# Performance work log

Hardware: AMD Instinct MI355X
Metric: run time of the kernel (lower is better)

The kernel has to match this reference:

```python
import jax, jax.numpy as jnp
import numpy as np

B, S, HID = 4, 512, 768
NH, HD = 12, 64          # num_heads, head_size = HID // NH
REL = 64                 # rel_dim
NEG_INF = -1e9


def setup_inputs() -> dict:
    key = jax.random.key(0)
    ks = jax.random.split(key, 12)
    input_tensor = jax.random.normal(ks[0], (B, S, HID), jnp.float32)
    graph_matrix = (jax.random.uniform(ks[1], (B, S, S)) < 0.3).astype(jnp.float32)
    # end_mask: one-hot at the last position (null attention slot)
    end_mask = jnp.zeros((B, S), jnp.float32).at[:, S - 1].set(1.0)
    rel_embeddings = jax.random.normal(ks[2], (B, S, S, REL), jnp.float32)
    w = lambda k, shp: jax.random.normal(k, shp, jnp.float32) * 0.02
    return {
        "input_tensor": input_tensor,
        "graph_matrix": graph_matrix,
        "end_mask": end_mask,
        "rel_embeddings": rel_embeddings,
        "Wq": w(ks[3], (HID, HID)), "bq": jnp.zeros((HID,), jnp.float32),
        "Wk": w(ks[4], (HID, HID)), "bk": jnp.zeros((HID,), jnp.float32),
        "Wv": w(ks[5], (HID, HID)), "bv": jnp.zeros((HID,), jnp.float32),
        "Wr": w(ks[6], (REL, HD)), "br": jnp.zeros((HD,), jnp.float32),
    }


def reference(input_tensor, graph_matrix, end_mask, rel_embeddings,
              Wq, bq, Wk, bk, Wv, bv, Wr, br):
    # use_null_att_pos: allow attending to the end/null slot
    g = graph_matrix + end_mask[:, None, :]              # (B,S,S)
    neg_inf_mask = (1.0 - g) * NEG_INF                   # (B,S,S)

    def heads(x):  # (B,S,HID) -> (B,NH,S,HD)
        return x.reshape(B, S, NH, HD).transpose(0, 2, 1, 3)

    q = heads(input_tensor @ Wq + bq)
    k = heads(input_tensor @ Wk + bk)
    v = heads(input_tensor @ Wv + bv)

    rel = rel_embeddings @ Wr + br                       # (B,S,S,HD), shared over heads
    # matmul_rel: (x_i * (y_j + z_ij)).sum(-1) = q.k^T + q.rel, per head
    scores = (jnp.einsum('bhid,bhjd->bhij', q, k)
              + jnp.einsum('bhid,bijd->bhij', q, rel))   # (B,NH,S,S)
    scores = scores / jnp.sqrt(jnp.float32(HD)) + neg_inf_mask[:, None]
    probs = jax.nn.softmax(scores, axis=-1)              # dropout p=0 -> identity

    ctx = jnp.einsum('bhij,bhjd->bhid', probs, v)        # (B,NH,S,HD)
    return ctx.transpose(0, 2, 1, 3).reshape(B, S, NH * HD)
```

## Files before the change

### kernel.cpp

```cpp
#include <hip/hip_runtime.h>
#include <hip/hip_bf16.h>
#include <hip/hip_fp16.h>
#include <cstddef>
#include <cstdint>

typedef __attribute__((ext_vector_type(8))) short bf16x8;
typedef __attribute__((ext_vector_type(4))) float f32x4;

#define MFMA16(a, b, c) __builtin_amdgcn_mfma_f32_16x16x32_bf16((a), (b), (c), 0, 0, 0)

static constexpr int B = 4, S = 512, HID = 768, NH = 12, HD = 64;
static constexpr int QKV_N = B * NH * S * HD;
static constexpr size_t SCORES_N = (size_t)B * NH * S * S;

__device__ __forceinline__ short f2bf(float f) {
  unsigned u = __builtin_bit_cast(unsigned, f);
  u += 0x7FFFu + ((u >> 16) & 1u);
  return (short)(u >> 16);
}
__device__ __forceinline__ float h2f(short s) {
  __half h = __builtin_bit_cast(__half, (unsigned short)s);
  return __half2float(h);
}
__device__ __forceinline__ bf16x8 ld_cvt8(const float* __restrict__ p) {
  float4 a = *reinterpret_cast<const float4*>(p);
  float4 b = *reinterpret_cast<const float4*>(p + 4);
  bf16x8 r;
  r[0] = f2bf(a.x); r[1] = f2bf(a.y); r[2] = f2bf(a.z); r[3] = f2bf(a.w);
  r[4] = f2bf(b.x); r[5] = f2bf(b.y); r[6] = f2bf(b.z); r[7] = f2bf(b.w);
  return r;
}
__device__ __forceinline__ f32x4 ld4nt(const float* p) {
  return __builtin_nontemporal_load(reinterpret_cast<const f32x4*>(p));
}
__device__ __forceinline__ bf16x8 cvt8(f32x4 a, f32x4 b) {
  bf16x8 r;
  r[0] = f2bf(a[0]); r[1] = f2bf(a[1]); r[2] = f2bf(a[2]); r[3] = f2bf(a[3]);
  r[4] = f2bf(b[0]); r[5] = f2bf(b[1]); r[6] = f2bf(b[2]); r[7] = f2bf(b[3]);
  return r;
}

__global__ __launch_bounds__(256) void k_qkv(
    const float* __restrict__ x,
    const float* __restrict__ Wq, const float* __restrict__ bq,
    const float* __restrict__ Wk, const float* __restrict__ bk,
    const float* __restrict__ Wv, const float* __restrict__ bv,
    const float* __restrict__ Wr,
    short* __restrict__ qkv, short* __restrict__ qrb, short* __restrict__ vT) {
  __shared__ short As[64 * 40];
  __shared__ short Bs[64 * 40];
  __shared__ short qs[64 * 72];
  const int m0 = blockIdx.x * 64;
  const int nt = blockIdx.y;
  const int mat = nt / 12;
  const int nc0 = (nt % 12) * 64;
  const float* __restrict__ W    = (mat == 0) ? Wq : (mat == 1) ? Wk : Wv;
  const float* __restrict__ bias = (mat == 0) ? bq : (mat == 1) ? bk : bv;
  short* __restrict__ outp = qkv + (size_t)mat * QKV_N;
  const int t = threadIdx.x;
  const int w = t >> 6, lane = t & 63;
  const int wm = (w >> 1) * 32, wn = (w & 1) * 32;
  const int lr = lane & 15, lk = lane >> 4;
  f32x4 acc[2][2] = {};
  for (int kk = 0; kk < 768; kk += 32) {
#pragma unroll
    for (int it = 0; it < 2; ++it) {
      int f = it * 256 + t;
      {
        int r = f >> 3, c4 = f & 7;
        float4 v = *reinterpret_cast<const float4*>(x + (size_t)(m0 + r) * 768 + kk + c4 * 4);
        short* d = &As[r * 40 + c4 * 4];
        d[0] = f2bf(v.x); d[1] = f2bf(v.y); d[2] = f2bf(v.z); d[3] = f2bf(v.w);
      }
      {
        int kr = f >> 4, c4 = f & 15;
        float4 v = *reinterpret_cast<const float4*>(W + (size_t)(kk + kr) * 768 + nc0 + c4 * 4);
        int c = c4 * 4;
        Bs[(c + 0) * 40 + kr] = f2bf(v.x);
        Bs[(c + 1) * 40 + kr] = f2bf(v.y);
        Bs[(c + 2) * 40 + kr] = f2bf(v.z);
        Bs[(c + 3) * 40 + kr] = f2bf(v.w);
      }
    }
    __syncthreads();
    bf16x8 a0 = *reinterpret_cast<const bf16x8*>(&As[(wm + lr) * 40 + lk * 8]);
    bf16x8 a1 = *reinterpret_cast<const bf16x8*>(&As[(wm + 16 + lr) * 40 + lk * 8]);
    bf16x8 b0 = *reinterpret_cast<const bf16x8*>(&Bs[(wn + lr) * 40 + lk * 8]);
    bf16x8 b1 = *reinterpret_cast<const bf16x8*>(&Bs[(wn + 16 + lr) * 40 + lk * 8]);
    acc[0][0] = MFMA16(a0, b0, acc[0][0]);
    acc[0][1] = MFMA16(a0, b1, acc[0][1]);
    acc[1][0] = MFMA16(a1, b0, acc[1][0]);
    acc[1][1] = MFMA16(a1, b1, acc[1][1]);
    __syncthreads();
  }
  const int b_ = m0 >> 9;
  if (mat == 2) {
#pragma unroll
    for (int mf = 0; mf < 2; ++mf)
#pragma unroll
      for (int nf = 0; nf < 2; ++nf) {
        int col = nc0 + wn + nf * 16 + lr;
        float bv_ = bias[col];
        int h = col >> 6, d = col & 63;
#pragma unroll
        for (int reg = 0; reg < 4; ++reg) {
          int j = (m0 + wm + mf * 16 + lk * 4 + reg) & 511;
          vT[((size_t)(b_ * NH + h) * HD + d) * S + j] = f2bf(acc[mf][nf][reg] + bv_);
        }
      }
    return;
  }
#pragma unroll
  for (int mf = 0; mf < 2; ++mf)
#pragma unroll
    for (int nf = 0; nf < 2; ++nf) {
      int col = nc0 + wn + nf * 16 + lr;
      float bv_ = bias[col];
      int h = col >> 6, d = col & 63;
#pragma unroll
      for (int reg = 0; reg < 4; ++reg) {
        int mloc = wm + mf * 16 + lk * 4 + reg;
        int i = (m0 + mloc) & 511;
        short qv = f2bf(acc[mf][nf][reg] + bv_);
        outp[(size_t)((b_ * NH + h) * S + i) * HD + d] = qv;
        if (mat == 0) qs[mloc * 72 + d] = qv;
      }
    }
  if (mat == 0) {
    const int h0 = nc0 >> 6;
    __syncthreads();
    f32x4 qacc[2][2] = {};
#pragma unroll
    for (int ks = 0; ks < 2; ++ks) {
      int k0 = ks * 32 + lk * 8;
      bf16x8 a0 = *reinterpret_cast<const bf16x8*>(&qs[(wm + lr) * 72 + k0]);
      bf16x8 a1 = *reinterpret_cast<const bf16x8*>(&qs[(wm + 16 + lr) * 72 + k0]);
      bf16x8 b0 = ld_cvt8(Wr + (size_t)(wn + lr) * 64 + k0);
      bf16x8 b1 = ld_cvt8(Wr + (size_t)(wn + 16 + lr) * 64 + k0);
      qacc[0][0] = MFMA16(a0, b0, qacc[0][0]);
      qacc[0][1] = MFMA16(a0, b1, qacc[0][1]);
      qacc[1][0] = MFMA16(a1, b0, qacc[1][0]);
      qacc[1][1] = MFMA16(a1, b1, qacc[1][1]);
    }
#pragma unroll
    for (int mf = 0; mf < 2; ++mf)
#pragma unroll
      for (int nf = 0; nf < 2; ++nf) {
        int r = wn + nf * 16 + lr;
#pragma unroll
        for (int reg = 0; reg < 4; ++reg) {
          int i = (m0 + wm + mf * 16 + lk * 4 + reg) & 511;
          qrb[((size_t)(b_ * NH + h0) * S + i) * 64 + r] = f2bf(qacc[mf][nf][reg] * 0.125f);
        }
      }
  }
}

__global__ __launch_bounds__(256) void k_qk(const short* __restrict__ q,
                                            const short* __restrict__ kmat,
                                            const float* __restrict__ graph,
                                            const float* __restrict__ endm,
                                            __half* __restrict__ sc) {
  const int j0 = blockIdx.x * 64, i0 = blockIdx.y * 64;
  const int bh = blockIdx.z;
  const int b = bh / NH, hh = bh % NH;
  const short* __restrict__ qp = q + (size_t)(bh * S) * HD;
  const short* __restrict__ kp = kmat + (size_t)(bh * S) * HD;
  const int t = threadIdx.x;
  const int w = t >> 6, lane = t & 63;
  const int wm = (w >> 1) * 32, wn = (w & 1) * 32;
  const int lr = lane & 15, lk = lane >> 4;
  f32x4 acc[2][2] = {};
#pragma unroll
  for (int ks = 0; ks < 2; ++ks) {
    int k0 = ks * 32 + lk * 8;
    bf16x8 a0 = *reinterpret_cast<const bf16x8*>(qp + (size_t)(i0 + wm + lr) * 64 + k0);
    bf16x8 a1 = *reinterpret_cast<const bf16x8*>(qp + (size_t)(i0 + wm + 16 + lr) * 64 + k0);
    bf16x8 b0 = *reinterpret_cast<const bf16x8*>(kp + (size_t)(j0 + wn + lr) * 64 + k0);
    bf16x8 b1 = *reinterpret_cast<const bf16x8*>(kp + (size_t)(j0 + wn + 16 + lr) * 64 + k0);
    acc[0][0] = MFMA16(a0, b0, acc[0][0]);
    acc[0][1] = MFMA16(a0, b1, acc[0][1]);
    acc[1][0] = MFMA16(a1, b0, acc[1][0]);
    acc[1][1] = MFMA16(a1, b1, acc[1][1]);
  }
#pragma unroll
  for (int mf = 0; mf < 2; ++mf)
#pragma unroll
    for (int nf = 0; nf < 2; ++nf) {
      int j = j0 + wn + nf * 16 + lr;
      float e = endm[b * S + j];
#pragma unroll
      for (int reg = 0; reg < 4; ++reg) {
        int i = i0 + wm + mf * 16 + lk * 4 + reg;
        float g = graph[(size_t)(b * S + i) * S + j];
        float s = acc[mf][nf][reg] * 0.125f + (1.0f - g - e) * (-30000.0f);
        sc[(((size_t)b * S + i) * NH + hh) * S + j] = __float2half(s);
      }
    }
}

__global__ __launch_bounds__(256) void k_relsm(const short* __restrict__ qrb,
                                               const float* __restrict__ rel,
                                               const __half* __restrict__ sc,
                                               short* __restrict__ probs) {
  __shared__ short sq[16 * 520];
  __shared__ float den_lds[64];
  const int i = blockIdx.x, b = blockIdx.y;
  const int t = threadIdx.x;
  const int w = t >> 6, lane = t & 63;
  const int lr = lane & 15, fq = lane >> 4;
  {
    const short* src = reinterpret_cast<const short*>(sc + ((size_t)(b * S) + i) * NH * S);
    int hh = t >> 4, js = (t & 15) * 32;
    const short* sp = src + (size_t)hh * S + js;
    short* dp = &sq[hh * 520 + js];
#pragma unroll
    for (int c = 0; c < 4; ++c)
      *reinterpret_cast<bf16x8*>(dp + c * 8) = *reinterpret_cast<const bf16x8*>(sp + c * 8);
  }
  const int hA = (lr < NH) ? lr : 0;
  const short* qrow = qrb + ((size_t)(b * NH + hA) * S + i) * 64;
  bf16x8 a0 = *reinterpret_cast<const bf16x8*>(qrow + fq * 8);
  bf16x8 a1 = *reinterpret_cast<const bf16x8*>(qrow + 32 + fq * 8);
  const float* rp = rel + (((size_t)(b * S) + i) * S + (size_t)(w * 128 + lr)) * 64 + fq * 8;
  float p[8][4];
  float den[4] = {0.f, 0.f, 0.f, 0.f};
  f32x4 c0 = ld4nt(rp), c1 = ld4nt(rp + 4), c2 = ld4nt(rp + 32), c3 = ld4nt(rp + 36);
  __syncthreads();
#pragma unroll
  for (int tt = 0; tt < 8; ++tt) {
    f32x4 n0, n1, n2, n3;
    if (tt < 7) {
      const float* rn = rp + (size_t)(tt + 1) * 1024;
      n0 = ld4nt(rn); n1 = ld4nt(rn + 4); n2 = ld4nt(rn + 32); n3 = ld4nt(rn + 36);
    }
    bf16x8 b0 = cvt8(c0, c1), b1 = cvt8(c2, c3);
    f32x4 acc = {};
    acc = MFMA16(a0, b0, acc);
    acc = MFMA16(a1, b1, acc);
    const int j0 = w * 128 + tt * 16;
#pragma unroll
    for (int r = 0; r < 4; ++r) {
      int h = fq * 4 + r;
      float s = acc[r] + h2f(sq[h * 520 + j0 + lr]);
      float pe = __expf(fminf(s, 80.0f));
      den[r] += pe;
      p[tt][r] = pe;
    }
    if (tt < 7) { c0 = n0; c1 = n1; c2 = n2; c3 = n3; }
  }
#pragma unroll
  for (int r = 0; r < 4; ++r) {
    float d = den[r];
    d += __shfl_xor(d, 1); d += __shfl_xor(d, 2);
    d += __shfl_xor(d, 4); d += __shfl_xor(d, 8);
    den[r] = d;
  }
  if (lr == 0) {
#pragma unroll
    for (int r = 0; r < 4; ++r) den_lds[w * 16 + fq * 4 + r] = den[r];
  }
  __syncthreads();
  float invd[4];
#pragma unroll
  for (int r = 0; r < 4; ++r) {
    int h = fq * 4 + r;
    invd[r] = 1.0f / (den_lds[h] + den_lds[16 + h] + den_lds[32 + h] + den_lds[48 + h]);
  }
#pragma unroll
  for (int tt = 0; tt < 8; ++tt) {
    int j0 = w * 128 + tt * 16;
#pragma unroll
    for (int r = 0; r < 4; ++r) {
      int h = fq * 4 + r;
      if (h < NH)
        probs[((size_t)(b * NH + h) * S + i) * S + j0 + lr] = f2bf(p[tt][r] * invd[r]);
    }
  }
}

__global__ __launch_bounds__(256) void k_pv2(const short* __restrict__ probs,
                                             const short* __restrict__ vT,
                                             float* __restrict__ out) {
  const int i0 = blockIdx.x * 32;
  const int h = blockIdx.y, b = blockIdx.z;
  const short* __restrict__ pp  = probs + (size_t)((b * NH + h) * S) * S;
  const short* __restrict__ vtp = vT + (size_t)((b * NH + h) * HD) * S;
  const int t = threadIdx.x;
  const int w = t >> 6, lane = t & 63;
  const int wm = (w >> 1) * 16, wn = (w & 1) * 32;
  const int lr = lane & 15, lk = lane >> 4;
  f32x4 acc[2] = {};
#pragma unroll
  for (int j0 = 0; j0 < S; j0 += 64) {
#pragma unroll
    for (int ks = 0; ks < 2; ++ks) {
      int k0 = j0 + ks * 32 + lk * 8;
      bf16x8 a0 = *reinterpret_cast<const bf16x8*>(pp + (size_t)(i0 + wm + lr) * S + k0);
      bf16x8 b0 = *reinterpret_cast<const bf16x8*>(vtp + (size_t)(wn + lr) * S + k0);
      bf16x8 b1 = *reinterpret_cast<const bf16x8*>(vtp + (size_t)(wn + 16 + lr) * S + k0);
      acc[0] = MFMA16(a0, b0, acc[0]);
      acc[1] = MFMA16(a0, b1, acc[1]);
    }
  }
#pragma unroll
  for (int nf = 0; nf < 2; ++nf) {
    int d = wn + nf * 16 + lr;
#pragma unroll
    for (int reg = 0; reg < 4; ++reg) {
      int i = i0 + wm + lk * 4 + reg;
      out[((size_t)(b * S) + i) * HID + h * 64 + d] = acc[nf][reg];
    }
  }
}

extern "C" void kernel_launch(void* const* d_in, const int* in_sizes, int n_in,
                              void* d_out, int out_size, void* d_ws, size_t ws_size,
                              hipStream_t stream) {
  const float* x     = (const float*)d_in[0];
  const float* graph = (const float*)d_in[1];
  const float* endm  = (const float*)d_in[2];
  const float* rel   = (const float*)d_in[3];
  const float* Wq = (const float*)d_in[4];  const float* bq = (const float*)d_in[5];
  const float* Wk = (const float*)d_in[6];  const float* bk = (const float*)d_in[7];
  const float* Wv = (const float*)d_in[8];  const float* bv = (const float*)d_in[9];
  const float* Wr = (const float*)d_in[10];

  short* qb  = (short*)d_ws;
  short* kb  = qb + QKV_N;
  short* vTb = kb + QKV_N;
  short* qrb = vTb + QKV_N;
  __half* scores = (__half*)(qrb + QKV_N);
  short* probs   = (short*)(scores + SCORES_N);
  const size_t need = (size_t)4 * QKV_N * 2 + SCORES_N * 2 + SCORES_N * 2;
  if (ws_size < need) return;

  k_qkv<<<dim3(32, 36), 256, 0, stream>>>(x, Wq, bq, Wk, bk, Wv, bv, Wr, qb, qrb, vTb);
  k_qk<<<dim3(8, 8, B * NH), 256, 0, stream>>>(qb, kb, graph, endm, scores);
  k_relsm<<<dim3(S, B), 256, 0, stream>>>(qrb, rel, scores, probs);
  k_pv2<<<dim3(16, NH, B), 256, 0, stream>>>(probs, vTb, (float*)d_out);
}
```

Baseline: 164.6 us.

## Precast inputs to bf16, pretranspose weights, fold Wr into Q projection

Adds a prep kernel that converts x to bf16, transposes Wq/Wk/Wv into bf16 K-major layout, and precomputes a combined Wq·Wr^T matrix (scaled) plus bias. The QKV GEMM then loads bf16 operands straight from global memory without LDS staging or barriers, and computes the q·rel projection as a fourth output matrix instead of a second chained MFMA pass. This removes per-tile fp32→bf16 conversion and the strided LDS transpose. The cost is an extra launch and workspace traffic, plus a slight change in rounding because Wr is folded into the weights before bf16 rounding.

New measurement: 200.7 us. +21.9%, slower.

```diff
diff --git a/kernel.cpp b/kernel.cpp
--- a/kernel.cpp
+++ b/kernel.cpp
@@ -12,6 +12,8 @@
 static constexpr int B = 4, S = 512, HID = 768, NH = 12, HD = 64;
 static constexpr int QKV_N = B * NH * S * HD;
 static constexpr size_t SCORES_N = (size_t)B * NH * S * S;
+static constexpr int XB_N  = 2048 * 768;
+static constexpr int WT_N  = 768 * 768;
 
 __device__ __forceinline__ short f2bf(float f) {
   unsigned u = __builtin_bit_cast(unsigned, f);
@@ -40,120 +42,135 @@
   return r;
 }
 
-__global__ __launch_bounds__(256) void k_qkv(
+__global__ __launch_bounds__(256) void k_prep(
     const float* __restrict__ x,
-    const float* __restrict__ Wq, const float* __restrict__ bq,
-    const float* __restrict__ Wk, const float* __restrict__ bk,
-    const float* __restrict__ Wv, const float* __restrict__ bv,
-    const float* __restrict__ Wr,
-    short* __restrict__ qkv, short* __restrict__ qrb, short* __restrict__ vT) {
-  __shared__ short As[64 * 40];
-  __shared__ short Bs[64 * 40];
-  __shared__ short qs[64 * 72];
-  const int m0 = blockIdx.x * 64;
-  const int nt = blockIdx.y;
-  const int mat = nt / 12;
-  const int nc0 = (nt % 12) * 64;
-  const float* __restrict__ W    = (mat == 0) ? Wq : (mat == 1) ? Wk : Wv;
-  const float* __restrict__ bias = (mat == 0) ? bq : (mat == 1) ? bk : bv;
-  short* __restrict__ outp = qkv + (size_t)mat * QKV_N;
-  const int t = threadIdx.x;
+    const float* __restrict__ Wq, const float* __restrict__ Wk,
+    const float* __restrict__ Wv, const float* __restrict__ Wr,
+    const float* __restrict__ bq,
+    short* __restrict__ xb, short* __restrict__ WbT,
+    short* __restrict__ WqrT, float* __restrict__ bqr) {
+  __shared__ short tile[64 * 72];
+  const int blk = blockIdx.x;
+  const int t = threadIdx.x;
+  if (blk < 768) {
+    size_t base = (size_t)blk * 2048 + t * 8;
+    *reinterpret_cast<bf16x8*>(xb + base) = ld_cvt8(x + base);
+    return;
+  }
+  if (blk < 1200) {
+    int q = blk - 768;
+    int mat = q / 144, rest = q % 144;
+    int kt = (rest / 12) * 64, nt = (rest % 12) * 64;
+    const float* __restrict__ W = (mat == 0) ? Wq : (mat == 1) ? Wk : Wv;
+    int r0 = t >> 2, c0 = (t & 3) * 16;
+    const float* src = W + (size_t)(kt + r0) * 768 + nt + c0;
+#pragma unroll
+    for (int u = 0; u < 16; u += 4) {
+      float4 v = *reinterpret_cast<const float4*>(src + u);
+      tile[(c0 + u + 0) * 72 + r0] = f2bf(v.x);
+      tile[(c0 + u + 1) * 72 + r0] = f2bf(v.y);
+      tile[(c0 + u + 2) * 72 + r0] = f2bf(v.z);
+      tile[(c0 + u + 3) * 72 + r0] = f2bf(v.w);
+    }
+    __syncthreads();
+    short* dst = WbT + (size_t)mat * WT_N + (size_t)(nt + r0) * 768 + kt + c0;
+    *reinterpret_cast<bf16x8*>(dst)     = *reinterpret_cast<const bf16x8*>(&tile[r0 * 72 + c0]);
+    *reinterpret_cast<bf16x8*>(dst + 8) = *reinterpret_cast<const bf16x8*>(&tile[r0 * 72 + c0 + 8]);
+    return;
+  }
+  const int h = blk - 1200;
+  if (t < 64) {
+    float s = 0.f;
+#pragma unroll
+    for (int d = 0; d < 64; ++d) s += bq[h * 64 + d] * Wr[t * 64 + d];
+    bqr[h * 64 + t] = 0.125f * s;
+  }
   const int w = t >> 6, lane = t & 63;
   const int wm = (w >> 1) * 32, wn = (w & 1) * 32;
   const int lr = lane & 15, lk = lane >> 4;
+  for (int kt = 0; kt < 768; kt += 64) {
+    f32x4 acc[2][2] = {};
+#pragma unroll
+    for (int ks = 0; ks < 2; ++ks) {
+      int d0 = ks * 32 + lk * 8;
+      bf16x8 a0 = ld_cvt8(Wr + (size_t)(wm + lr) * 64 + d0);
+      bf16x8 a1 = ld_cvt8(Wr + (size_t)(wm + 16 + lr) * 64 + d0);
+      bf16x8 b0 = ld_cvt8(Wq + (size_t)(kt + wn + lr) * 768 + h * 64 + d0);
+      bf16x8 b1 = ld_cvt8(Wq + (size_t)(kt + wn + 16 + lr) * 768 + h * 64 + d0);
+      acc[0][0] = MFMA16(a0, b0, acc[0][0]);
+      acc[0][1] = MFMA16(a0, b1, acc[0][1]);
+      acc[1][0] = MFMA16(a1, b0, acc[1][0]);
+      acc[1][1] = MFMA16(a1, b1, acc[1][1]);
+    }
+#pragma unroll
+    for (int mf = 0; mf < 2; ++mf)
+#pragma unroll
+      for (int nf = 0; nf < 2; ++nf) {
+        int kcol = kt + wn + nf * 16 + lr;
+#pragma unroll
+        for (int reg = 0; reg < 4; ++reg) {
+          int r = wm + mf * 16 + lk * 4 + reg;
+          WqrT[(size_t)(h * 64 + r) * 768 + kcol] = f2bf(0.125f * acc[mf][nf][reg]);
+        }
+      }
+  }
+}
+
+__global__ __launch_bounds__(256) void k_qkv2(
+    const short* __restrict__ xb, const short* __restrict__ WbT,
+    const short* __restrict__ WqrT,
+    const float* __restrict__ bq, const float* __restrict__ bk,
+    const float* __restrict__ bv, const float* __restrict__ bqr,
+    short* __restrict__ qkv, short* __restrict__ qrb, short* __restrict__ vT) {
+  const int m0 = blockIdx.x * 64;
+  const int nb = blockIdx.y;
+  const int mat = nb / 12, h0 = nb % 12;
+  const short* __restrict__ Bp =
+      (mat < 3) ? WbT + (size_t)mat * WT_N + (size_t)(h0 * 64) * 768
+                : WqrT + (size_t)(h0 * 64) * 768;
+  const float* __restrict__ bias =
+      (mat == 0) ? bq + h0 * 64 : (mat == 1) ? bk + h0 * 64
+      : (mat == 2) ? bv + h0 * 64 : bqr + h0 * 64;
+  const int t = threadIdx.x;
+  const int w = t >> 6, lane = t & 63;
+  const int wm = (w >> 1) * 32, wn = (w & 1) * 32;
+  const int lr = lane & 15, lk = lane >> 4;
+  const short* ap0 = xb + (size_t)(m0 + wm + lr) * 768 + lk * 8;
+  const short* ap1 = xb + (size_t)(m0 + wm + 16 + lr) * 768 + lk * 8;
+  const short* bp0 = Bp + (size_t)(wn + lr) * 768 + lk * 8;
+  const short* bp1 = Bp + (size_t)(wn + 16 + lr) * 768 + lk * 8;
   f32x4 acc[2][2] = {};
+#pragma unroll 2
   for (int kk = 0; kk < 768; kk += 32) {
-#pragma unroll
-    for (int it = 0; it < 2; ++it) {
-      int f = it * 256 + t;
-      {
-        int r = f >> 3, c4 = f & 7;
-        float4 v = *reinterpret_cast<const float4*>(x + (size_t)(m0 + r) * 768 + kk + c4 * 4);
-        short* d = &As[r * 40 + c4 * 4];
-        d[0] = f2bf(v.x); d[1] = f2bf(v.y); d[2] = f2bf(v.z); d[3] = f2bf(v.w);
-      }
-      {
-        int kr = f >> 4, c4 = f & 15;
-        float4 v = *reinterpret_cast<const float4*>(W + (size_t)(kk + kr) * 768 + nc0 + c4 * 4);
-        int c = c4 * 4;
-        Bs[(c + 0) * 40 + kr] = f2bf(v.x);
-        Bs[(c + 1) * 40 + kr] = f2bf(v.y);
-        Bs[(c + 2) * 40 + kr] = f2bf(v.z);
-        Bs[(c + 3) * 40 + kr] = f2bf(v.w);
-      }
-    }
-    __syncthreads();
-    bf16x8 a0 = *reinterpret_cast<const bf16x8*>(&As[(wm + lr) * 40 + lk * 8]);
-    bf16x8 a1 = *reinterpret_cast<const bf16x8*>(&As[(wm + 16 + lr) * 40 + lk * 8]);
-    bf16x8 b0 = *reinterpret_cast<const bf16x8*>(&Bs[(wn + lr) * 40 + lk * 8]);
-    bf16x8 b1 = *reinterpret_cast<const bf16x8*>(&Bs[(wn + 16 + lr) * 40 + lk * 8]);
+    bf16x8 a0 = *reinterpret_cast<const bf16x8*>(ap0 + kk);
+    bf16x8 a1 = *reinterpret_cast<const bf16x8*>(ap1 + kk);
+    bf16x8 b0 = *reinterpret_cast<const bf16x8*>(bp0 + kk);
+    bf16x8 b1 = *reinterpret_cast<const bf16x8*>(bp1 + kk);
     acc[0][0] = MFMA16(a0, b0, acc[0][0]);
     acc[0][1] = MFMA16(a0, b1, acc[0][1]);
     acc[1][0] = MFMA16(a1, b0, acc[1][0]);
     acc[1][1] = MFMA16(a1, b1, acc[1][1]);
-    __syncthreads();
   }
   const int b_ = m0 >> 9;
-  if (mat == 2) {
-#pragma unroll
-    for (int mf = 0; mf < 2; ++mf)
-#pragma unroll
-      for (int nf = 0; nf < 2; ++nf) {
-        int col = nc0 + wn + nf * 16 + lr;
-        float bv_ = bias[col];
-        int h = col >> 6, d = col & 63;
-#pragma unroll
-        for (int reg = 0; reg < 4; ++reg) {
-          int j = (m0 + wm + mf * 16 + lk * 4 + reg) & 511;
-          vT[((size_t)(b_ * NH + h) * HD + d) * S + j] = f2bf(acc[mf][nf][reg] + bv_);
+#pragma unroll
+  for (int mf = 0; mf < 2; ++mf)
+#pragma unroll
+    for (int nf = 0; nf < 2; ++nf) {
+      int d = wn + nf * 16 + lr;
+      float bv_ = bias[d];
+#pragma unroll
+      for (int reg = 0; reg < 4; ++reg) {
+        int i = (m0 + wm + mf * 16 + lk * 4 + reg) & 511;
+        float val = acc[mf][nf][reg] + bv_;
+        if (mat == 2) {
+          vT[((size_t)(b_ * NH + h0) * HD + d) * S + i] = f2bf(val);
+        } else if (mat == 3) {
+          qrb[((size_t)(b_ * NH + h0) * S + i) * 64 + d] = f2bf(val);
+        } else {
+          qkv[(size_t)mat * QKV_N + (size_t)((b_ * NH + h0) * S + i) * HD + d] = f2bf(val);
         }
       }
-    return;
-  }
-#pragma unroll
-  for (int mf = 0; mf < 2; ++mf)
-#pragma unroll
-    for (int nf = 0; nf < 2; ++nf) {
-      int col = nc0 + wn + nf * 16 + lr;
-      float bv_ = bias[col];
-      int h = col >> 6, d = col & 63;
-#pragma unroll
-      for (int reg = 0; reg < 4; ++reg) {
-        int mloc = wm + mf * 16 + lk * 4 + reg;
-        int i = (m0 + mloc) & 511;
-        short qv = f2bf(acc[mf][nf][reg] + bv_);
-        outp[(size_t)((b_ * NH + h) * S + i) * HD + d] = qv;
-        if (mat == 0) qs[mloc * 72 + d] = qv;
-      }
-    }
-  if (mat == 0) {
-    const int h0 = nc0 >> 6;
-    __syncthreads();
-    f32x4 qacc[2][2] = {};
-#pragma unroll
-    for (int ks = 0; ks < 2; ++ks) {
-      int k0 = ks * 32 + lk * 8;
-      bf16x8 a0 = *reinterpret_cast<const bf16x8*>(&qs[(wm + lr) * 72 + k0]);
-      bf16x8 a1 = *reinterpret_cast<const bf16x8*>(&qs[(wm + 16 + lr) * 72 + k0]);
-      bf16x8 b0 = ld_cvt8(Wr + (size_t)(wn + lr) * 64 + k0);
-      bf16x8 b1 = ld_cvt8(Wr + (size_t)(wn + 16 + lr) * 64 + k0);
-      qacc[0][0] = MFMA16(a0, b0, qacc[0][0]);
-      qacc[0][1] = MFMA16(a0, b1, qacc[0][1]);
-      qacc[1][0] = MFMA16(a1, b0, qacc[1][0]);
-      qacc[1][1] = MFMA16(a1, b1, qacc[1][1]);
-    }
-#pragma unroll
-    for (int mf = 0; mf < 2; ++mf)
-#pragma unroll
-      for (int nf = 0; nf < 2; ++nf) {
-        int r = wn + nf * 16 + lr;
-#pragma unroll
-        for (int reg = 0; reg < 4; ++reg) {
-          int i = (m0 + wm + mf * 16 + lk * 4 + reg) & 511;
-          qrb[((size_t)(b_ * NH + h0) * S + i) * 64 + r] = f2bf(qacc[mf][nf][reg] * 0.125f);
-        }
-      }
-  }
+    }
 }
 
 __global__ __launch_bounds__(256) void k_qk(const short* __restrict__ q,
@@ -326,16 +343,22 @@
   const float* Wv = (const float*)d_in[8];  const float* bv = (const float*)d_in[9];
   const float* Wr = (const float*)d_in[10];
 
-  short* qb  = (short*)d_ws;
-  short* kb  = qb + QKV_N;
-  short* vTb = kb + QKV_N;
-  short* qrb = vTb + QKV_N;
+  short* xb   = (short*)d_ws;
+  short* WbT  = xb + XB_N;
+  short* WqrT = WbT + 3 * WT_N;
+  float* bqr  = (float*)(WqrT + WT_N);
+  short* qb   = (short*)(bqr + 768);
+  short* kb   = qb + QKV_N;
+  short* vTb  = kb + QKV_N;
+  short* qrb  = vTb + QKV_N;
   __half* scores = (__half*)(qrb + QKV_N);
   short* probs   = (short*)(scores + SCORES_N);
-  const size_t need = (size_t)4 * QKV_N * 2 + SCORES_N * 2 + SCORES_N * 2;
+  const size_t need = (size_t)(XB_N + 4 * WT_N) * 2 + 768 * 4 +
+                      (size_t)4 * QKV_N * 2 + SCORES_N * 2 + SCORES_N * 2;
   if (ws_size < need) return;
 
-  k_qkv<<<dim3(32, 36), 256, 0, stream>>>(x, Wq, bq, Wk, bk, Wv, bv, Wr, qb, qrb, vTb);
+  k_prep<<<dim3(1212), 256, 0, stream>>>(x, Wq, Wk, Wv, Wr, bq, xb, WbT, WqrT, bqr);
+  k_qkv2<<<dim3(32, 48), 256, 0, stream>>>(xb, WbT, WqrT, bq, bk, bv, bqr, qb, qrb, vTb);
   k_qk<<<dim3(8, 8, B * NH), 256, 0, stream>>>(qb, kb, graph, endm, scores);
   k_relsm<<<dim3(S, B), 256, 0, stream>>>(qrb, rel, scores, probs);
   k_pv2<<<dim3(16, NH, B), 256, 0, stream>>>(probs, vTb, (float*)d_out);
```
